# Optimization experiments

Measured on AMD Instinct MI355X. Metric: run time of the kernel, lower is better.

Reference implementation:

```python
import jax, jax.numpy as jnp
import numpy as np

NUM_HEADS = 16
NUM_KV_HEADS = 4
HEAD_DIM = 64
HIDDEN = 1024
R_SOFTPLUS_0 = 1.442695041


def setup_inputs() -> dict:
    key = jax.random.key(0)
    ks = jax.random.split(key, 6)
    B, S = 2, 2048
    qkv_out = (NUM_HEADS + 2 * NUM_KV_HEADS) * HEAD_DIM  # 1536
    return {
        "hidden_states": jax.random.normal(ks[0], (B, S, HIDDEN), dtype=jnp.float32),
        "scaling": jax.random.normal(ks[1], (HEAD_DIM,), dtype=jnp.float32),
        "qkv_w": jax.random.normal(ks[2], (qkv_out, HIDDEN), dtype=jnp.float32) * (1.0 / np.sqrt(HIDDEN)),
        "qkv_b": jax.random.normal(ks[3], (qkv_out,), dtype=jnp.float32) * 0.01,
        "o_w": jax.random.normal(ks[4], (HIDDEN, NUM_HEADS * HEAD_DIM), dtype=jnp.float32) * (1.0 / np.sqrt(NUM_HEADS * HEAD_DIM)),
        "o_b": jax.random.normal(ks[5], (HIDDEN,), dtype=jnp.float32) * 0.01,
    }


def reference(hidden_states, scaling, qkv_w, qkv_b, o_w, o_b):
    B, S, _ = hidden_states.shape
    H, KV, D = NUM_HEADS, NUM_KV_HEADS, HEAD_DIM
    rep = H // KV

    qkv = hidden_states @ qkv_w.T + qkv_b  # [B,S,(H+2KV)*D]
    xq, xk, xv = jnp.split(qkv, [H * D, H * D + KV * D], axis=-1)
    xq = xq.reshape(B, S, H, D)
    xk = xk.reshape(B, S, KV, D)
    xv = xv.reshape(B, S, KV, D)

    # per-dim softplus scaling of queries
    scale = (R_SOFTPLUS_0 / jnp.sqrt(jnp.float32(D))) * jax.nn.softplus(scaling)
    xq = xq * scale[None, None, None, :]

    # GQA: repeat kv heads to match query heads
    xk = jnp.repeat(xk, rep, axis=2)  # [B,S,H,D]
    xv = jnp.repeat(xv, rep, axis=2)

    scores = jnp.einsum("bqhd,bkhd->bhqk", xq, xk)  # [B,H,S,S]
    probs = jax.nn.softmax(scores.astype(jnp.float32), axis=-1).astype(xq.dtype)
    out = jnp.einsum("bhqk,bkhd->bqhd", probs, xv)  # [B,S,H,D]
    out = out.reshape(B, S, H * D)
    return out @ o_w.T + o_b
```

## Files before the change

### kernel.cpp

```cpp
#include <hip/hip_runtime.h>
#include <stdint.h>

#define HQ 16
#define HKV 4
#define DH 64
#define HID 1024
#define QKVN 1536
#define SEQ 2048
#define NB 2
#define NTOK 4096

typedef __bf16 bf16x8 __attribute__((ext_vector_type(8)));
typedef __bf16 bf16x2 __attribute__((ext_vector_type(2)));
typedef float f32x4 __attribute__((ext_vector_type(4)));
typedef float f32x16 __attribute__((ext_vector_type(16)));
typedef unsigned int u32;
typedef unsigned short u16;

__device__ __forceinline__ u32 pk(float lo, float hi) {
  bf16x2 t;
  t[0] = (__bf16)lo;
  t[1] = (__bf16)hi;
  return __builtin_bit_cast(u32, t);
}
__device__ __forceinline__ u16 bf1(float f) {
  return __builtin_bit_cast(u16, (__bf16)f);
}

__device__ __forceinline__ void gl_lds16(const void* g, void* l) {
  __builtin_amdgcn_global_load_lds(
      (__attribute__((address_space(1))) u32*)(uintptr_t)g,
      (__attribute__((address_space(3))) u32*)(u32)(uintptr_t)l, 16, 0, 0);
}

#if __has_builtin(__builtin_amdgcn_exp2f)
#define EXP2(x) __builtin_amdgcn_exp2f(x)
#else
#define EXP2(x) __expf((x) * 0.69314718055994531f)
#endif

#if __has_builtin(__builtin_amdgcn_fdot2_f32_bf16)
#define HAVE_DOT2 1
#endif

#define FENCE() asm volatile("" ::: "memory")

__global__ void cvt_bf16_kernel(const float* __restrict__ h,
                                const float* __restrict__ w1,
                                const float* __restrict__ w2,
                                u16* __restrict__ oh, u16* __restrict__ ow1,
                                u16* __restrict__ ow2) {
  const int NH = NTOK * HID / 8, NW1 = QKVN * HID / 8, NW2 = HID * HID / 8;
  int idx = blockIdx.x * blockDim.x + threadIdx.x;
  if (idx >= NH + NW1 + NW2) return;
  const float* s; u16* d; int o;
  if (idx < NH) { s = h; d = oh; o = idx; }
  else if (idx < NH + NW1) { s = w1; d = ow1; o = idx - NH; }
  else { s = w2; d = ow2; o = idx - NH - NW1; }
  const float4* sp = (const float4*)s + (size_t)o * 2;
  float4 a = sp[0], b = sp[1];
  uint4 out;
  out.x = pk(a.x, a.y);
  out.y = pk(a.z, a.w);
  out.z = pk(b.x, b.y);
  out.w = pk(b.z, b.w);
  *((uint4*)(d + (size_t)o * 8)) = out;
}

template <int EPI>
__global__ __launch_bounds__(256, 3) void gemm_nt_kernel(
    const u16* __restrict__ A, const u16* __restrict__ Bw,
    const float* __restrict__ bias, const float* __restrict__ scaling,
    void* __restrict__ Out, int ldout) {
  constexpr int BM = 64;
  constexpr int MR = BM / 32;
  constexpr int ACH = BM / 32;
  constexpr int BUF = BM * 128 + 16384;
  __shared__ char smem[2 * BUF];
  const int tid = threadIdx.x;
  const int lane = tid & 63, wid = tid >> 6;
  const int l15 = lane & 15, lg = lane >> 4;
  const int wr = wid >> 1, wc = wid & 1;
  const int mt = blockIdx.x * BM, nt = blockIdx.y * 128;

  const u16* ag[ACH]; const u16* bg[4]; int al[ACH]; int bl[4];
#pragma unroll
  for (int c = 0; c < ACH; c++) {
    int chunk = wid * ACH + c;
    int rp = chunk * 8 + (lane >> 3);
    int lb = (lane & 7) ^ (rp & 7);
    ag[c] = A + (size_t)(mt + rp) * HID + lb * 8;
    al[c] = chunk * 1024;
  }
#pragma unroll
  for (int c = 0; c < 4; c++) {
    int chunk = wid * 4 + c;
    int rp = chunk * 8 + (lane >> 3);
    int lb = (lane & 7) ^ (rp & 7);
    bg[c] = Bw + (size_t)(nt + rp) * HID + lb * 8;
    bl[c] = BM * 128 + chunk * 1024;
  }

  f32x4 acc[MR][4] = {};

#pragma unroll
  for (int c = 0; c < ACH; c++) gl_lds16(ag[c], smem + al[c]);
#pragma unroll
  for (int c = 0; c < 4; c++) gl_lds16(bg[c], smem + bl[c]);

  for (int kt = 0; kt < HID / 64; kt++) {
    const int cur = (kt & 1) * BUF;
    const int nxt = BUF - cur;
    if (kt < HID / 64 - 1) {
#pragma unroll
      for (int c = 0; c < ACH; c++) gl_lds16(ag[c] + (kt + 1) * 64, smem + nxt + al[c]);
#pragma unroll
      for (int c = 0; c < 4; c++) gl_lds16(bg[c] + (kt + 1) * 64, smem + nxt + bl[c]);
      asm volatile("s_waitcnt vmcnt(6)" ::: "memory");
    } else {
      asm volatile("s_waitcnt vmcnt(0)" ::: "memory");
    }
    __builtin_amdgcn_s_barrier();
    FENCE();
    const char* Asm = smem + cur;
    const char* Bsm = smem + cur + BM * 128;
#pragma unroll
    for (int kk = 0; kk < 2; kk++) {
      bf16x8 af[MR], bfr[4];
#pragma unroll
      for (int mi = 0; mi < MR; mi++) {
        int row = wr * (BM / 2) + mi * 16 + l15;
        int blk = kk * 4 + lg;
        af[mi] = *(const bf16x8*)(Asm + row * 128 + ((blk ^ (row & 7)) << 4));
      }
#pragma unroll
      for (int nj = 0; nj < 4; nj++) {
        int row = wc * 64 + nj * 16 + l15;
        int blk = kk * 4 + lg;
        bfr[nj] = *(const bf16x8*)(Bsm + row * 128 + ((blk ^ (row & 7)) << 4));
      }
#pragma unroll
      for (int mi = 0; mi < MR; mi++)
#pragma unroll
        for (int nj = 0; nj < 4; nj++)
          acc[mi][nj] = __builtin_amdgcn_mfma_f32_16x16x32_bf16(af[mi], bfr[nj],
                                                                acc[mi][nj], 0, 0, 0);
    }
    FENCE();
    __builtin_amdgcn_s_barrier();
    FENCE();
  }

  if (EPI == 0) {
    float qs[4];
#pragma unroll
    for (int nj = 0; nj < 4; nj++) {
      int col = nt + wc * 64 + nj * 16 + l15;
      if (col < HQ * DH) {
        float x = scaling[col & 63];
        float sp = (x > 15.f) ? x : log1pf(__expf(x));
        qs[nj] = (1.442695041f / 8.0f) * sp * 1.442695041f;
      } else {
        qs[nj] = 1.0f;
      }
    }
    u16* O = (u16*)Out;
#pragma unroll
    for (int mi = 0; mi < MR; mi++)
#pragma unroll
      for (int nj = 0; nj < 4; nj++)
#pragma unroll
        for (int r = 0; r < 4; r++) {
          int row = mt + wr * (BM / 2) + mi * 16 + lg * 4 + r;
          int col = nt + wc * 64 + nj * 16 + l15;
          float v = (acc[mi][nj][r] + bias[col]) * qs[nj];
          O[(size_t)row * ldout + col] = bf1(v);
        }
  } else {
    float* O = (float*)Out;
#pragma unroll
    for (int mi = 0; mi < MR; mi++)
#pragma unroll
      for (int nj = 0; nj < 4; nj++)
#pragma unroll
        for (int r = 0; r < 4; r++) {
          int row = mt + wr * (BM / 2) + mi * 16 + lg * 4 + r;
          int col = nt + wc * 64 + nj * 16 + l15;
          O[(size_t)row * ldout + col] = acc[mi][nj][r] + bias[col];
        }
  }
}

__global__ __launch_bounds__(256) void vtrans_kernel(const u16* __restrict__ qkv,
                                                     u16* __restrict__ vt) {
  __shared__ u16 tile[64][68];
  int tt = blockIdx.x;
  int g = blockIdx.y;
  int b = g >> 2, kv = g & 3;
  int ts = tt * 64;
  int t = threadIdx.x;
#pragma unroll
  for (int pass = 0; pass < 4; pass++) {
    int tok = pass * 16 + (t >> 4);
    int d0 = (t & 15) * 4;
    const u16* src = qkv + (size_t)(b * SEQ + ts + tok) * QKVN + (HQ * DH + HKV * DH) + kv * DH + d0;
    *(uint2*)&tile[tok][d0] = *(const uint2*)src;
  }
  __syncthreads();
#pragma unroll
  for (int pass = 0; pass < 16; pass++) {
    int flat = pass * 256 + t;
    int d = flat >> 6, tok = flat & 63;
    vt[(size_t)(g * 64 + d) * SEQ + ts + tok] = tile[tok][d];
  }
}

__global__ __launch_bounds__(512, 4) void attn_kernel(const u16* __restrict__ qkv,
                                                      const u16* __restrict__ vt,
                                                      u16* __restrict__ aout) {
  __shared__ char smem[65536];
  const int tid = threadIdx.x, lane = tid & 63, wid = tid >> 6;
  const int l31 = lane & 31, hi = lane >> 5;
  const int g = wid >> 2, wg = wid & 3;
  const int kvb = g * 1024;
  const int qt = blockIdx.x, bh = blockIdx.y;
  const int b = bh >> 4, h = bh & 15, kvh = h >> 2;
  const int tb = b * SEQ;

  bf16x8 qb[4];
  const int qrow_g = tb + qt * 128 + wg * 32 + l31;
#pragma unroll
  for (int kk = 0; kk < 4; kk++)
    qb[kk] = *(const bf16x8*)(qkv + (size_t)qrow_g * QKVN + h * DH + kk * 16 + hi * 8);

  const int rsub = lane >> 3;
  const int gsw = ((lane & 7) ^ rsub) * 8;
  const u16* kgb[2]; const u16* vgb[2]; int klo[2], vlo[2];
#pragma unroll
  for (int c = 0; c < 2; c++) {
    int ch = wg * 2 + c;
    int rp = ch * 8 + rsub;
    int ktok = (rp & ~12) | ((rp & 4) << 1) | ((rp & 8) >> 1);
    kgb[c] = qkv + (size_t)(tb + kvb + ktok) * QKVN + HQ * DH + kvh * DH + gsw;
    vgb[c] = vt + (size_t)((b * HKV + kvh) * DH + rp) * SEQ + kvb + gsw;
    klo[c] = g * 16384 + ch * 1024;
    vlo[c] = g * 16384 + 8192 + ch * 1024;
  }

  f32x16 ot0 = {}, ot1 = {};
  float l_run = 0.f;

#pragma unroll
  for (int c = 0; c < 2; c++) {
    gl_lds16(kgb[c], smem + klo[c]);
    gl_lds16(vgb[c], smem + vlo[c]);
    kgb[c] += 64 * QKVN;
    vgb[c] += 64;
  }

  const int swz = l31 & 7;

  for (int kt = 0; kt < 16; kt++) {
    const int cur = (kt & 1) * 32768;
    const int nxt = 32768 - cur;
    if (kt < 15) {
#pragma unroll
      for (int c = 0; c < 2; c++) {
        gl_lds16(kgb[c], smem + nxt + klo[c]);
        gl_lds16(vgb[c], smem + nxt + vlo[c]);
        kgb[c] += 64 * QKVN;
        vgb[c] += 64;
      }
      asm volatile("s_waitcnt vmcnt(4)" ::: "memory");
    } else {
      asm volatile("s_waitcnt vmcnt(0)" ::: "memory");
    }
    __builtin_amdgcn_s_barrier();
    FENCE();

    const char* Ks = smem + cur + g * 16384;
    const char* Vs = Ks + 8192;

    f32x16 s0 = {}, s1 = {};
#pragma unroll
    for (int kk = 0; kk < 4; kk++) {
      int gp = kk * 2 + hi;
      bf16x8 ka0 = *(const bf16x8*)(Ks + l31 * 128 + ((gp ^ swz) << 4));
      bf16x8 ka1 = *(const bf16x8*)(Ks + (l31 + 32) * 128 + ((gp ^ swz) << 4));
      s0 = __builtin_amdgcn_mfma_f32_32x32x16_bf16(ka0, qb[kk], s0, 0, 0, 0);
      s1 = __builtin_amdgcn_mfma_f32_32x32x16_bf16(ka1, qb[kk], s1, 0, 0, 0);
    }

#pragma unroll
    for (int i = 0; i < 16; i++) s0[i] = EXP2(s0[i]);
#pragma unroll
    for (int i = 0; i < 16; i++) s1[i] = EXP2(s1[i]);

    float lsum = 0.f;
#ifndef HAVE_DOT2
    {
      float ts[16];
#pragma unroll
      for (int i = 0; i < 16; i++) ts[i] = s0[i] + s1[i];
#pragma unroll
      for (int st = 8; st > 0; st >>= 1)
#pragma unroll
        for (int i = 0; i < 8; i++)
          if (i < st) ts[i] += ts[i + st];
      lsum = ts[0];
    }
#endif
#ifdef HAVE_DOT2
    const bf16x2 ones2 = {(__bf16)1.0f, (__bf16)1.0f};
#endif
#pragma unroll
    for (int ck = 0; ck < 4; ck++) {
      float p[8];
#pragma unroll
      for (int j = 0; j < 8; j++)
        p[j] = (ck < 2) ? s0[(ck & 1) * 8 + j] : s1[(ck & 1) * 8 + j];
      union { u32 u[4]; bf16x8 v; } pu;
      pu.u[0] = pk(p[0], p[1]);
      pu.u[1] = pk(p[2], p[3]);
      pu.u[2] = pk(p[4], p[5]);
      pu.u[3] = pk(p[6], p[7]);
#ifdef HAVE_DOT2
#pragma unroll
      for (int w = 0; w < 4; w++)
        lsum = __builtin_amdgcn_fdot2_f32_bf16(
            __builtin_bit_cast(bf16x2, pu.u[w]), ones2, lsum, false);
#endif
      int gp = ck * 2 + hi;
      bf16x8 va0 = *(const bf16x8*)(Vs + l31 * 128 + ((gp ^ swz) << 4));
      bf16x8 va1 = *(const bf16x8*)(Vs + (l31 + 32) * 128 + ((gp ^ swz) << 4));
      ot0 = __builtin_amdgcn_mfma_f32_32x32x16_bf16(va0, pu.v, ot0, 0, 0, 0);
      ot1 = __builtin_amdgcn_mfma_f32_32x32x16_bf16(va1, pu.v, ot1, 0, 0, 0);
    }
    l_run += lsum + __shfl_xor(lsum, 32);
    FENCE();
    __builtin_amdgcn_s_barrier();
    FENCE();
  }

  __syncthreads();
  if (wid >= 4) {
    int idx = tid - 256;
    float* ex0 = (float*)smem;
    float* ex1 = (float*)(smem + 16384);
#pragma unroll
    for (int j = 0; j < 16; j++) ex0[j * 256 + idx] = ot0[j];
#pragma unroll
    for (int j = 0; j < 16; j++) ex1[j * 256 + idx] = ot1[j];
    ((float*)(smem + 32768))[idx] = l_run;
  }
  __syncthreads();
  if (wid < 4) {
    const float* ex0 = (const float*)smem;
    const float* ex1 = (const float*)(smem + 16384);
    l_run += ((const float*)(smem + 32768))[tid];
#pragma unroll
    for (int j = 0; j < 16; j++) ot0[j] += ex0[j * 256 + tid];
#pragma unroll
    for (int j = 0; j < 16; j++) ot1[j] += ex1[j * 256 + tid];
  }
  __syncthreads();

  u16* Ot = (u16*)(smem + 36864);
  if (wid < 4) {
    float inv = 1.0f / l_run;
    const int qrow_l = wg * 32 + l31;
#pragma unroll
    for (int dt = 0; dt < 2; dt++)
#pragma unroll
      for (int rq = 0; rq < 4; rq++) {
        int d0 = dt * 32 + rq * 8 + 4 * hi;
        float v0, v1, v2, v3;
        if (dt == 0) {
          v0 = ot0[rq * 4 + 0]; v1 = ot0[rq * 4 + 1]; v2 = ot0[rq * 4 + 2]; v3 = ot0[rq * 4 + 3];
        } else {
          v0 = ot1[rq * 4 + 0]; v1 = ot1[rq * 4 + 1]; v2 = ot1[rq * 4 + 2]; v3 = ot1[rq * 4 + 3];
        }
        u32 wa = pk(v0 * inv, v1 * inv);
        u32 wb = pk(v2 * inv, v3 * inv);
        int ga = ((d0 >> 3) ^ (qrow_l & 7));
        *(u32*)((char*)Ot + qrow_l * 128 + ga * 16 + ((d0 & 7) << 1)) = wa;
        *(u32*)((char*)Ot + qrow_l * 128 + ga * 16 + (((d0 + 2) & 7) << 1)) = wb;
      }
  }
  __syncthreads();
#pragma unroll
  for (int it = 0; it < 2; it++) {
    int gidx = it * 512 + tid;
    int row = gidx >> 3, c8 = gidx & 7;
    int pos = c8 ^ (row & 7);
    uint4 val = *(const uint4*)((const char*)Ot + row * 128 + pos * 16);
    *(uint4*)(aout + (size_t)(tb + qt * 128 + row) * (HQ * DH) + h * DH + c8 * 8) = val;
  }
}

extern "C" void kernel_launch(void* const* d_in, const int* in_sizes, int n_in,
                              void* d_out, int out_size, void* d_ws, size_t ws_size,
                              hipStream_t stream) {
  const float* hs = (const float*)d_in[0];
  const float* scaling = (const float*)d_in[1];
  const float* qkv_w = (const float*)d_in[2];
  const float* qkv_b = (const float*)d_in[3];
  const float* o_w = (const float*)d_in[4];
  const float* o_b = (const float*)d_in[5];
  float* out = (float*)d_out;

  char* ws = (char*)d_ws;
  u16* h_bf = (u16*)ws;
  u16* w1_bf = (u16*)(ws + 8388608);
  u16* w2_bf = (u16*)(ws + 11534336);
  u16* qkv = (u16*)(ws + 13631488);
  u16* vtb = (u16*)(ws + 26214400);
  u16* att = (u16*)(ws + 28311552);

  {
    int tot = (NTOK * HID + QKVN * HID + HID * HID) / 8;
    cvt_bf16_kernel<<<(tot + 255) / 256, 256, 0, stream>>>(hs, qkv_w, o_w, h_bf, w1_bf, w2_bf);
  }
  gemm_nt_kernel<0><<<dim3(NTOK / 64, QKVN / 128), 256, 0, stream>>>(
      h_bf, w1_bf, qkv_b, scaling, qkv, QKVN);
  vtrans_kernel<<<dim3(SEQ / 64, NB * HKV), 256, 0, stream>>>(qkv, vtb);
  attn_kernel<<<dim3(SEQ / 128, NB * HQ), 512, 0, stream>>>(qkv, vtb, att);
  gemm_nt_kernel<1><<<dim3(NTOK / 64, HID / 128), 256, 0, stream>>>(
      att, w2_bf, o_b, nullptr, out, HID);
}
```

Measured before the change: 83.47 us.

## Process two 32-row query chunks per wave to double K/V reuse in attention

Each wave now holds two 32-row query chunks, so an attention block covers 256 queries instead of 128 and the grid is halved. Each K and V fragment read from shared memory feeds twice as many MFMAs, and each block loads K/V from global memory once for twice the queries. The cost is roughly double the accumulator registers: launch bounds drop from 4 to 2 blocks per CU, occupancy falls, and only 256 blocks launch. The cross-group reduction at the end is split into two rounds to fit in shared memory.

```diff
diff --git a/kernel.cpp b/kernel.cpp
--- a/kernel.cpp
+++ b/kernel.cpp
@@ -215,7 +215,7 @@
   }
 }
 
-__global__ __launch_bounds__(512, 4) void attn_kernel(const u16* __restrict__ qkv,
+__global__ __launch_bounds__(512, 2) void attn_kernel(const u16* __restrict__ qkv,
                                                       const u16* __restrict__ vt,
                                                       u16* __restrict__ aout) {
   __shared__ char smem[65536];
@@ -227,11 +227,14 @@
   const int b = bh >> 4, h = bh & 15, kvh = h >> 2;
   const int tb = b * SEQ;
 
-  bf16x8 qb[4];
-  const int qrow_g = tb + qt * 128 + wg * 32 + l31;
-#pragma unroll
-  for (int kk = 0; kk < 4; kk++)
-    qb[kk] = *(const bf16x8*)(qkv + (size_t)qrow_g * QKVN + h * DH + kk * 16 + hi * 8);
+  bf16x8 qb[2][4];
+#pragma unroll
+  for (int qc = 0; qc < 2; qc++)
+#pragma unroll
+    for (int kk = 0; kk < 4; kk++) {
+      int row = tb + qt * 256 + wg * 64 + qc * 32 + l31;
+      qb[qc][kk] = *(const bf16x8*)(qkv + (size_t)row * QKVN + h * DH + kk * 16 + hi * 8);
+    }
 
   const int rsub = lane >> 3;
   const int gsw = ((lane & 7) ^ rsub) * 8;
@@ -247,8 +250,8 @@
     vlo[c] = g * 16384 + 8192 + ch * 1024;
   }
 
-  f32x16 ot0 = {}, ot1 = {};
-  float l_run = 0.f;
+  f32x16 ot[2][2] = {};
+  float l_run[2] = {0.f, 0.f};
 
 #pragma unroll
   for (int c = 0; c < 2; c++) {
@@ -281,120 +284,142 @@
     const char* Ks = smem + cur + g * 16384;
     const char* Vs = Ks + 8192;
 
-    f32x16 s0 = {}, s1 = {};
+    f32x16 s[2][2] = {};
 #pragma unroll
     for (int kk = 0; kk < 4; kk++) {
       int gp = kk * 2 + hi;
       bf16x8 ka0 = *(const bf16x8*)(Ks + l31 * 128 + ((gp ^ swz) << 4));
       bf16x8 ka1 = *(const bf16x8*)(Ks + (l31 + 32) * 128 + ((gp ^ swz) << 4));
-      s0 = __builtin_amdgcn_mfma_f32_32x32x16_bf16(ka0, qb[kk], s0, 0, 0, 0);
-      s1 = __builtin_amdgcn_mfma_f32_32x32x16_bf16(ka1, qb[kk], s1, 0, 0, 0);
-    }
-
-#pragma unroll
-    for (int i = 0; i < 16; i++) s0[i] = EXP2(s0[i]);
-#pragma unroll
-    for (int i = 0; i < 16; i++) s1[i] = EXP2(s1[i]);
-
-    float lsum = 0.f;
-#ifndef HAVE_DOT2
-    {
-      float ts[16];
-#pragma unroll
-      for (int i = 0; i < 16; i++) ts[i] = s0[i] + s1[i];
-#pragma unroll
-      for (int st = 8; st > 0; st >>= 1)
-#pragma unroll
-        for (int i = 0; i < 8; i++)
-          if (i < st) ts[i] += ts[i + st];
-      lsum = ts[0];
-    }
-#endif
+#pragma unroll
+      for (int qc = 0; qc < 2; qc++) {
+        s[qc][0] = __builtin_amdgcn_mfma_f32_32x32x16_bf16(ka0, qb[qc][kk], s[qc][0], 0, 0, 0);
+        s[qc][1] = __builtin_amdgcn_mfma_f32_32x32x16_bf16(ka1, qb[qc][kk], s[qc][1], 0, 0, 0);
+      }
+    }
+
+#pragma unroll
+    for (int qc = 0; qc < 2; qc++)
+#pragma unroll
+      for (int hf = 0; hf < 2; hf++)
+#pragma unroll
+        for (int i = 0; i < 16; i++) s[qc][hf][i] = EXP2(s[qc][hf][i]);
+
+    float lsum[2] = {0.f, 0.f};
 #ifdef HAVE_DOT2
     const bf16x2 ones2 = {(__bf16)1.0f, (__bf16)1.0f};
 #endif
+#ifndef HAVE_DOT2
+#pragma unroll
+    for (int qc = 0; qc < 2; qc++) {
+      float ts[16];
+#pragma unroll
+      for (int i = 0; i < 16; i++) ts[i] = s[qc][0][i] + s[qc][1][i];
+#pragma unroll
+      for (int st = 8; st > 0; st >>= 1)
+#pragma unroll
+        for (int i = 0; i < 8; i++)
+          if (i < st) ts[i] += ts[i + st];
+      lsum[qc] = ts[0];
+    }
+#endif
 #pragma unroll
     for (int ck = 0; ck < 4; ck++) {
-      float p[8];
-#pragma unroll
-      for (int j = 0; j < 8; j++)
-        p[j] = (ck < 2) ? s0[(ck & 1) * 8 + j] : s1[(ck & 1) * 8 + j];
-      union { u32 u[4]; bf16x8 v; } pu;
-      pu.u[0] = pk(p[0], p[1]);
-      pu.u[1] = pk(p[2], p[3]);
-      pu.u[2] = pk(p[4], p[5]);
-      pu.u[3] = pk(p[6], p[7]);
-#ifdef HAVE_DOT2
-#pragma unroll
-      for (int w = 0; w < 4; w++)
-        lsum = __builtin_amdgcn_fdot2_f32_bf16(
-            __builtin_bit_cast(bf16x2, pu.u[w]), ones2, lsum, false);
-#endif
       int gp = ck * 2 + hi;
       bf16x8 va0 = *(const bf16x8*)(Vs + l31 * 128 + ((gp ^ swz) << 4));
       bf16x8 va1 = *(const bf16x8*)(Vs + (l31 + 32) * 128 + ((gp ^ swz) << 4));
-      ot0 = __builtin_amdgcn_mfma_f32_32x32x16_bf16(va0, pu.v, ot0, 0, 0, 0);
-      ot1 = __builtin_amdgcn_mfma_f32_32x32x16_bf16(va1, pu.v, ot1, 0, 0, 0);
-    }
-    l_run += lsum + __shfl_xor(lsum, 32);
+#pragma unroll
+      for (int qc = 0; qc < 2; qc++) {
+        const int hf = (ck < 2) ? 0 : 1;
+        const int base = (ck & 1) * 8;
+        union { u32 u[4]; bf16x8 v; } pu;
+        pu.u[0] = pk(s[qc][hf][base + 0], s[qc][hf][base + 1]);
+        pu.u[1] = pk(s[qc][hf][base + 2], s[qc][hf][base + 3]);
+        pu.u[2] = pk(s[qc][hf][base + 4], s[qc][hf][base + 5]);
+        pu.u[3] = pk(s[qc][hf][base + 6], s[qc][hf][base + 7]);
+#ifdef HAVE_DOT2
+#pragma unroll
+        for (int w = 0; w < 4; w++)
+          lsum[qc] = __builtin_amdgcn_fdot2_f32_bf16(
+              __builtin_bit_cast(bf16x2, pu.u[w]), ones2, lsum[qc], false);
+#endif
+        ot[qc][0] = __builtin_amdgcn_mfma_f32_32x32x16_bf16(va0, pu.v, ot[qc][0], 0, 0, 0);
+        ot[qc][1] = __builtin_amdgcn_mfma_f32_32x32x16_bf16(va1, pu.v, ot[qc][1], 0, 0, 0);
+      }
+    }
+#pragma unroll
+    for (int qc = 0; qc < 2; qc++)
+      l_run[qc] += lsum[qc] + __shfl_xor(lsum[qc], 32);
     FENCE();
     __builtin_amdgcn_s_barrier();
     FENCE();
   }
 
+  float* exf = (float*)smem;
   __syncthreads();
   if (wid >= 4) {
     int idx = tid - 256;
-    float* ex0 = (float*)smem;
-    float* ex1 = (float*)(smem + 16384);
-#pragma unroll
-    for (int j = 0; j < 16; j++) ex0[j * 256 + idx] = ot0[j];
-#pragma unroll
-    for (int j = 0; j < 16; j++) ex1[j * 256 + idx] = ot1[j];
-    ((float*)(smem + 32768))[idx] = l_run;
+#pragma unroll
+    for (int j = 0; j < 16; j++) exf[j * 256 + idx] = ot[0][0][j];
+#pragma unroll
+    for (int j = 0; j < 16; j++) exf[(16 + j) * 256 + idx] = ot[0][1][j];
+    ((float*)(smem + 32768))[idx] = l_run[0];
+    ((float*)(smem + 33792))[idx] = l_run[1];
   }
   __syncthreads();
   if (wid < 4) {
-    const float* ex0 = (const float*)smem;
-    const float* ex1 = (const float*)(smem + 16384);
-    l_run += ((const float*)(smem + 32768))[tid];
-#pragma unroll
-    for (int j = 0; j < 16; j++) ot0[j] += ex0[j * 256 + tid];
-#pragma unroll
-    for (int j = 0; j < 16; j++) ot1[j] += ex1[j * 256 + tid];
-  }
-  __syncthreads();
-
-  u16* Ot = (u16*)(smem + 36864);
+#pragma unroll
+    for (int j = 0; j < 16; j++) ot[0][0][j] += exf[j * 256 + tid];
+#pragma unroll
+    for (int j = 0; j < 16; j++) ot[0][1][j] += exf[(16 + j) * 256 + tid];
+    l_run[0] += ((const float*)(smem + 32768))[tid];
+    l_run[1] += ((const float*)(smem + 33792))[tid];
+  }
+  __syncthreads();
+  if (wid >= 4) {
+    int idx = tid - 256;
+#pragma unroll
+    for (int j = 0; j < 16; j++) exf[j * 256 + idx] = ot[1][0][j];
+#pragma unroll
+    for (int j = 0; j < 16; j++) exf[(16 + j) * 256 + idx] = ot[1][1][j];
+  }
+  __syncthreads();
   if (wid < 4) {
-    float inv = 1.0f / l_run;
-    const int qrow_l = wg * 32 + l31;
-#pragma unroll
-    for (int dt = 0; dt < 2; dt++)
-#pragma unroll
-      for (int rq = 0; rq < 4; rq++) {
-        int d0 = dt * 32 + rq * 8 + 4 * hi;
-        float v0, v1, v2, v3;
-        if (dt == 0) {
-          v0 = ot0[rq * 4 + 0]; v1 = ot0[rq * 4 + 1]; v2 = ot0[rq * 4 + 2]; v3 = ot0[rq * 4 + 3];
-        } else {
-          v0 = ot1[rq * 4 + 0]; v1 = ot1[rq * 4 + 1]; v2 = ot1[rq * 4 + 2]; v3 = ot1[rq * 4 + 3];
+#pragma unroll
+    for (int j = 0; j < 16; j++) ot[1][0][j] += exf[j * 256 + tid];
+#pragma unroll
+    for (int j = 0; j < 16; j++) ot[1][1][j] += exf[(16 + j) * 256 + tid];
+  }
+  __syncthreads();
+
+  u16* Ot = (u16*)smem;
+  if (wid < 4) {
+#pragma unroll
+    for (int qc = 0; qc < 2; qc++) {
+      float inv = 1.0f / l_run[qc];
+      const int qrow_l = wg * 64 + qc * 32 + l31;
+#pragma unroll
+      for (int hf = 0; hf < 2; hf++)
+#pragma unroll
+        for (int rq = 0; rq < 4; rq++) {
+          int d0 = hf * 32 + rq * 8 + 4 * hi;
+          float v0 = ot[qc][hf][rq * 4 + 0], v1 = ot[qc][hf][rq * 4 + 1];
+          float v2 = ot[qc][hf][rq * 4 + 2], v3 = ot[qc][hf][rq * 4 + 3];
+          u32 wa = pk(v0 * inv, v1 * inv);
+          u32 wb = pk(v2 * inv, v3 * inv);
+          int ga = ((d0 >> 3) ^ (qrow_l & 7));
+          *(u32*)((char*)Ot + qrow_l * 128 + ga * 16 + ((d0 & 7) << 1)) = wa;
+          *(u32*)((char*)Ot + qrow_l * 128 + ga * 16 + (((d0 + 2) & 7) << 1)) = wb;
         }
-        u32 wa = pk(v0 * inv, v1 * inv);
-        u32 wb = pk(v2 * inv, v3 * inv);
-        int ga = ((d0 >> 3) ^ (qrow_l & 7));
-        *(u32*)((char*)Ot + qrow_l * 128 + ga * 16 + ((d0 & 7) << 1)) = wa;
-        *(u32*)((char*)Ot + qrow_l * 128 + ga * 16 + (((d0 + 2) & 7) << 1)) = wb;
-      }
-  }
-  __syncthreads();
-#pragma unroll
-  for (int it = 0; it < 2; it++) {
+    }
+  }
+  __syncthreads();
+#pragma unroll
+  for (int it = 0; it < 4; it++) {
     int gidx = it * 512 + tid;
     int row = gidx >> 3, c8 = gidx & 7;
     int pos = c8 ^ (row & 7);
     uint4 val = *(const uint4*)((const char*)Ot + row * 128 + pos * 16);
-    *(uint4*)(aout + (size_t)(tb + qt * 128 + row) * (HQ * DH) + h * DH + c8 * 8) = val;
+    *(uint4*)(aout + (size_t)(tb + qt * 256 + row) * (HQ * DH) + h * DH + c8 * 8) = val;
   }
 }
 
@@ -424,7 +449,7 @@
   gemm_nt_kernel<0><<<dim3(NTOK / 64, QKVN / 128), 256, 0, stream>>>(
       h_bf, w1_bf, qkv_b, scaling, qkv, QKVN);
   vtrans_kernel<<<dim3(SEQ / 64, NB * HKV), 256, 0, stream>>>(qkv, vtb);
-  attn_kernel<<<dim3(SEQ / 128, NB * HQ), 512, 0, stream>>>(qkv, vtb, att);
+  attn_kernel<<<dim3(SEQ / 256, NB * HQ), 512, 0, stream>>>(qkv, vtb, att);
   gemm_nt_kernel<1><<<dim3(NTOK / 64, HID / 128), 256, 0, stream>>>(
       att, w2_bf, o_b, nullptr, out, HID);
 }
```

Result: faster. 81.23 us (-2.7%).

## Fuse V transpose into QKV GEMM and deepen attention K/V pipeline

Applied to the files above, without the earlier changes.

Removes the separate V-transpose kernel. The QKV GEMM epilogue now also writes V columns transposed straight into the vt buffer. The attention kernel moves from 64-token tiles double-buffered to 32-token tiles in a 4-stage ring with prefetch distance 2, using a new V LDS layout and swizzle. Barriers now wait only on lgkmcnt with a sched_barrier instead of a full fence. This saves one launch and extra memory traffic, but the transposed V stores in the GEMM epilogue are scattered and the attention loop takes more, smaller iterations.

```diff
diff --git a/kernel.cpp b/kernel.cpp
--- a/kernel.cpp
+++ b/kernel.cpp
@@ -71,7 +71,7 @@
 __global__ __launch_bounds__(256, 3) void gemm_nt_kernel(
     const u16* __restrict__ A, const u16* __restrict__ Bw,
     const float* __restrict__ bias, const float* __restrict__ scaling,
-    void* __restrict__ Out, int ldout) {
+    void* __restrict__ Out, int ldout, u16* __restrict__ vt) {
   constexpr int BM = 64;
   constexpr int MR = BM / 32;
   constexpr int ACH = BM / 32;
@@ -146,7 +146,8 @@
           acc[mi][nj] = __builtin_amdgcn_mfma_f32_16x16x32_bf16(af[mi], bfr[nj],
                                                                 acc[mi][nj], 0, 0, 0);
     }
-    FENCE();
+    asm volatile("s_waitcnt lgkmcnt(0)" ::: "memory");
+    __builtin_amdgcn_sched_barrier(0);
     __builtin_amdgcn_s_barrier();
     FENCE();
   }
@@ -176,6 +177,22 @@
           float v = (acc[mi][nj][r] + bias[col]) * qs[nj];
           O[(size_t)row * ldout + col] = bf1(v);
         }
+    if (nt >= (HQ + HKV) * DH) {
+#pragma unroll
+      for (int mi = 0; mi < MR; mi++)
+#pragma unroll
+        for (int nj = 0; nj < 4; nj++)
+#pragma unroll
+          for (int r = 0; r < 4; r++) {
+            int row = mt + wr * (BM / 2) + mi * 16 + lg * 4 + r;
+            int col = nt + wc * 64 + nj * 16 + l15;
+            int vc = col - (HQ + HKV) * DH;
+            int kv = vc >> 6, d = vc & 63;
+            int b = row >> 11, tok = row & (SEQ - 1);
+            float v = acc[mi][nj][r] + bias[col];
+            vt[((size_t)(b * HKV + kv) * DH + d) * SEQ + tok] = bf1(v);
+          }
+    }
   } else {
     float* O = (float*)Out;
 #pragma unroll
@@ -191,32 +208,8 @@
   }
 }
 
-__global__ __launch_bounds__(256) void vtrans_kernel(const u16* __restrict__ qkv,
-                                                     u16* __restrict__ vt) {
-  __shared__ u16 tile[64][68];
-  int tt = blockIdx.x;
-  int g = blockIdx.y;
-  int b = g >> 2, kv = g & 3;
-  int ts = tt * 64;
-  int t = threadIdx.x;
-#pragma unroll
-  for (int pass = 0; pass < 4; pass++) {
-    int tok = pass * 16 + (t >> 4);
-    int d0 = (t & 15) * 4;
-    const u16* src = qkv + (size_t)(b * SEQ + ts + tok) * QKVN + (HQ * DH + HKV * DH) + kv * DH + d0;
-    *(uint2*)&tile[tok][d0] = *(const uint2*)src;
-  }
-  __syncthreads();
-#pragma unroll
-  for (int pass = 0; pass < 16; pass++) {
-    int flat = pass * 256 + t;
-    int d = flat >> 6, tok = flat & 63;
-    vt[(size_t)(g * 64 + d) * SEQ + ts + tok] = tile[tok][d];
-  }
-}
-
 __global__ __launch_bounds__(512, 4) void attn_kernel(const u16* __restrict__ qkv,
-                                                      const u16* __restrict__ vt,
+                                                      const u16* __restrict__ vtb,
                                                       u16* __restrict__ aout) {
   __shared__ char smem[65536];
   const int tid = threadIdx.x, lane = tid & 63, wid = tid >> 6;
@@ -226,6 +219,7 @@
   const int qt = blockIdx.x, bh = blockIdx.y;
   const int b = bh >> 4, h = bh & 15, kvh = h >> 2;
   const int tb = b * SEQ;
+  const int NT = 32;
 
   bf16x8 qb[4];
   const int qrow_g = tb + qt * 128 + wg * 32 + l31;
@@ -233,111 +227,91 @@
   for (int kk = 0; kk < 4; kk++)
     qb[kk] = *(const bf16x8*)(qkv + (size_t)qrow_g * QKVN + h * DH + kk * 16 + hi * 8);
 
-  const int rsub = lane >> 3;
-  const int gsw = ((lane & 7) ^ rsub) * 8;
-  const u16* kgb[2]; const u16* vgb[2]; int klo[2], vlo[2];
-#pragma unroll
-  for (int c = 0; c < 2; c++) {
-    int ch = wg * 2 + c;
-    int rp = ch * 8 + rsub;
-    int ktok = (rp & ~12) | ((rp & 4) << 1) | ((rp & 8) >> 1);
-    kgb[c] = qkv + (size_t)(tb + kvb + ktok) * QKVN + HQ * DH + kvh * DH + gsw;
-    vgb[c] = vt + (size_t)((b * HKV + kvh) * DH + rp) * SEQ + kvb + gsw;
-    klo[c] = g * 16384 + ch * 1024;
-    vlo[c] = g * 16384 + 8192 + ch * 1024;
+  const u16* kg; const u16* vg; int klo, vlo;
+  {
+    int krow = wg * 8 + (lane >> 3);
+    int kd = ((lane & 7) ^ (krow & 7)) * 8;
+    int ktok = (krow & ~12) | ((krow & 4) << 1) | ((krow & 8) >> 1);
+    kg = qkv + (size_t)(tb + kvb + ktok) * QKVN + HQ * DH + kvh * DH + kd;
+    klo = g * 8192 + wg * 1024;
+    int vR = wg * 8 + (lane >> 3);
+    int vp = (lane & 7) ^ (vR & 7);
+    int vd = 2 * vR + (vp >> 2);
+    int vgb = vp & 3;
+    vg = vtb + (size_t)((b * HKV + kvh) * DH + vd) * SEQ + kvb + vgb * 8;
+    vlo = g * 8192 + 4096 + wg * 1024;
   }
 
   f32x16 ot0 = {}, ot1 = {};
   float l_run = 0.f;
 
 #pragma unroll
-  for (int c = 0; c < 2; c++) {
-    gl_lds16(kgb[c], smem + klo[c]);
-    gl_lds16(vgb[c], smem + vlo[c]);
-    kgb[c] += 64 * QKVN;
-    vgb[c] += 64;
-  }
-
-  const int swz = l31 & 7;
-
-  for (int kt = 0; kt < 16; kt++) {
-    const int cur = (kt & 1) * 32768;
-    const int nxt = 32768 - cur;
-    if (kt < 15) {
-#pragma unroll
-      for (int c = 0; c < 2; c++) {
-        gl_lds16(kgb[c], smem + nxt + klo[c]);
-        gl_lds16(vgb[c], smem + nxt + vlo[c]);
-        kgb[c] += 64 * QKVN;
-        vgb[c] += 64;
-      }
+  for (int t = 0; t < 2; t++) {
+    gl_lds16(kg, smem + t * 16384 + klo);
+    gl_lds16(vg, smem + t * 16384 + vlo);
+    kg += 32 * QKVN;
+    vg += 32;
+  }
+
+  const int kswz = l31 & 7;
+
+  for (int kt = 0; kt < NT; kt++) {
+    if (kt + 2 < NT) {
+      const int stb = ((kt + 2) & 3) * 16384;
+      gl_lds16(kg, smem + stb + klo);
+      gl_lds16(vg, smem + stb + vlo);
+      kg += 32 * QKVN;
+      vg += 32;
       asm volatile("s_waitcnt vmcnt(4)" ::: "memory");
+    } else if (kt + 1 < NT) {
+      asm volatile("s_waitcnt vmcnt(2)" ::: "memory");
     } else {
       asm volatile("s_waitcnt vmcnt(0)" ::: "memory");
     }
     __builtin_amdgcn_s_barrier();
     FENCE();
 
-    const char* Ks = smem + cur + g * 16384;
-    const char* Vs = Ks + 8192;
-
-    f32x16 s0 = {}, s1 = {};
+    const char* Ks = smem + (kt & 3) * 16384 + g * 8192;
+    const char* Vs = Ks + 4096;
+
+    f32x16 s = {};
 #pragma unroll
     for (int kk = 0; kk < 4; kk++) {
-      int gp = kk * 2 + hi;
-      bf16x8 ka0 = *(const bf16x8*)(Ks + l31 * 128 + ((gp ^ swz) << 4));
-      bf16x8 ka1 = *(const bf16x8*)(Ks + (l31 + 32) * 128 + ((gp ^ swz) << 4));
-      s0 = __builtin_amdgcn_mfma_f32_32x32x16_bf16(ka0, qb[kk], s0, 0, 0, 0);
-      s1 = __builtin_amdgcn_mfma_f32_32x32x16_bf16(ka1, qb[kk], s1, 0, 0, 0);
-    }
-
-#pragma unroll
-    for (int i = 0; i < 16; i++) s0[i] = EXP2(s0[i]);
-#pragma unroll
-    for (int i = 0; i < 16; i++) s1[i] = EXP2(s1[i]);
+      bf16x8 ka = *(const bf16x8*)(Ks + l31 * 128 + (((kk * 2 + hi) ^ kswz) << 4));
+      s = __builtin_amdgcn_mfma_f32_32x32x16_bf16(ka, qb[kk], s, 0, 0, 0);
+    }
+
+#pragma unroll
+    for (int i = 0; i < 16; i++) s[i] = EXP2(s[i]);
 
     float lsum = 0.f;
-#ifndef HAVE_DOT2
-    {
-      float ts[16];
-#pragma unroll
-      for (int i = 0; i < 16; i++) ts[i] = s0[i] + s1[i];
-#pragma unroll
-      for (int st = 8; st > 0; st >>= 1)
-#pragma unroll
-        for (int i = 0; i < 8; i++)
-          if (i < st) ts[i] += ts[i + st];
-      lsum = ts[0];
-    }
-#endif
 #ifdef HAVE_DOT2
     const bf16x2 ones2 = {(__bf16)1.0f, (__bf16)1.0f};
+#else
+#pragma unroll
+    for (int i = 0; i < 16; i++) lsum += s[i];
 #endif
 #pragma unroll
-    for (int ck = 0; ck < 4; ck++) {
-      float p[8];
-#pragma unroll
-      for (int j = 0; j < 8; j++)
-        p[j] = (ck < 2) ? s0[(ck & 1) * 8 + j] : s1[(ck & 1) * 8 + j];
-      union { u32 u[4]; bf16x8 v; } pu;
-      pu.u[0] = pk(p[0], p[1]);
-      pu.u[1] = pk(p[2], p[3]);
-      pu.u[2] = pk(p[4], p[5]);
-      pu.u[3] = pk(p[6], p[7]);
+    for (int kb = 0; kb < 2; kb++) {
+      const int vsw = ((l31 & 1) * 4 + kb * 2 + hi) ^ ((l31 >> 1) & 7);
+      bf16x8 va0 = *(const bf16x8*)(Vs + (l31 >> 1) * 128 + (vsw << 4));
+      bf16x8 va1 = *(const bf16x8*)(Vs + (16 + (l31 >> 1)) * 128 + (vsw << 4));
+      union { u32 u[4]; bf16x8 v; } pa;
+#pragma unroll
+      for (int w = 0; w < 4; w++)
+        pa.u[w] = pk(s[kb * 8 + 2 * w], s[kb * 8 + 2 * w + 1]);
 #ifdef HAVE_DOT2
 #pragma unroll
       for (int w = 0; w < 4; w++)
-        lsum = __builtin_amdgcn_fdot2_f32_bf16(
-            __builtin_bit_cast(bf16x2, pu.u[w]), ones2, lsum, false);
+        lsum = __builtin_amdgcn_fdot2_f32_bf16(__builtin_bit_cast(bf16x2, pa.u[w]),
+                                               ones2, lsum, false);
 #endif
-      int gp = ck * 2 + hi;
-      bf16x8 va0 = *(const bf16x8*)(Vs + l31 * 128 + ((gp ^ swz) << 4));
-      bf16x8 va1 = *(const bf16x8*)(Vs + (l31 + 32) * 128 + ((gp ^ swz) << 4));
-      ot0 = __builtin_amdgcn_mfma_f32_32x32x16_bf16(va0, pu.v, ot0, 0, 0, 0);
-      ot1 = __builtin_amdgcn_mfma_f32_32x32x16_bf16(va1, pu.v, ot1, 0, 0, 0);
+      ot0 = __builtin_amdgcn_mfma_f32_32x32x16_bf16(va0, pa.v, ot0, 0, 0, 0);
+      ot1 = __builtin_amdgcn_mfma_f32_32x32x16_bf16(va1, pa.v, ot1, 0, 0, 0);
     }
     l_run += lsum + __shfl_xor(lsum, 32);
-    FENCE();
+    asm volatile("s_waitcnt lgkmcnt(0)" ::: "memory");
+    __builtin_amdgcn_sched_barrier(0);
     __builtin_amdgcn_s_barrier();
     FENCE();
   }
@@ -365,10 +339,10 @@
   }
   __syncthreads();
 
-  u16* Ot = (u16*)(smem + 36864);
+  u16* Ot = (u16*)smem;
   if (wid < 4) {
     float inv = 1.0f / l_run;
-    const int qrow_l = wg * 32 + l31;
+    const int qrow_l = wid * 32 + l31;
 #pragma unroll
     for (int dt = 0; dt < 2; dt++)
 #pragma unroll
@@ -422,9 +396,8 @@
     cvt_bf16_kernel<<<(tot + 255) / 256, 256, 0, stream>>>(hs, qkv_w, o_w, h_bf, w1_bf, w2_bf);
   }
   gemm_nt_kernel<0><<<dim3(NTOK / 64, QKVN / 128), 256, 0, stream>>>(
-      h_bf, w1_bf, qkv_b, scaling, qkv, QKVN);
-  vtrans_kernel<<<dim3(SEQ / 64, NB * HKV), 256, 0, stream>>>(qkv, vtb);
+      h_bf, w1_bf, qkv_b, scaling, qkv, QKVN, vtb);
   attn_kernel<<<dim3(SEQ / 128, NB * HQ), 512, 0, stream>>>(qkv, vtb, att);
   gemm_nt_kernel<1><<<dim3(NTOK / 64, HID / 128), 256, 0, stream>>>(
-      att, w2_bf, o_b, nullptr, out, HID);
-}
+      att, w2_bf, o_b, nullptr, out, HID, nullptr);
+}
```

After: 83.96 us. Within noise of the previous version (+0.6%).
